# Optimization experiments

Hardware: AMD Instinct MI355X
Metric: run time of the kernel (lower is better)

The kernel has to match this reference:

```python
import jax, jax.numpy as jnp
import numpy as np

# Code / decoder configuration (regular (3,6) QC-LDPC, rate 1/2)
B, N, M, E, ITERS = 128, 24576, 12288, 73728, 10
CN_DEG = 6          # check-node degree (E = M * CN_DEG, and each VN has degree 3)
CLIP = 20.0         # clip_llr (q_bit == 0 -> clamp with straight-through gradient)
BIG = jnp.float32(1e30)  # acts as +inf for segment-min init


def _quantize(llr):
    """q_bit == 0: clamp to [-CLIP, CLIP] with straight-through estimator."""
    q = jnp.clip(llr, -CLIP, CLIP)
    return jax.lax.stop_gradient(q) + (llr - jax.lax.stop_gradient(llr))


def _decode(llr_in, cn_weight, ch_weight, cn_bias, edge_to_vn, edge_to_cn):
    c2v = jnp.zeros((B, E), jnp.float32)
    sum_llr = jnp.zeros((B, N), jnp.float32)
    dec = llr_in
    loss = jnp.float32(0.0)
    for it in range(ITERS):
        # --- channel weight (sharing[2] == 3: per-iteration scalar) ---
        w_ch = llr_in * ch_weight[it]
        # --- VN update: extrinsic sum at each variable node, gathered per edge ---
        v2c = _quantize(w_ch[:, edge_to_vn] + sum_llr[:, edge_to_vn] - c2v)
        # --- CN update (min-sum): per-CN sign parity + extrinsic min via min1/min2 ---
        a = jnp.abs(v2c)                      # [B, E]
        neg = v2c < 0
        parity = jnp.zeros((B, M), jnp.int32).at[:, edge_to_cn].add(neg.astype(jnp.int32)) % 2
        sign_tot = (1 - 2 * parity).astype(jnp.float32)          # [B, M]
        m1 = jnp.full((B, M), BIG, jnp.float32).at[:, edge_to_cn].min(a)
        is_min = a == m1[:, edge_to_cn]
        cnt = jnp.zeros((B, M), jnp.float32).at[:, edge_to_cn].add(is_min.astype(jnp.float32))
        m2 = jnp.full((B, M), BIG, jnp.float32).at[:, edge_to_cn].min(jnp.where(is_min, BIG, a))
        # edge is the unique minimum of its CN -> use second min; otherwise first min
        ext_min = jnp.where(is_min & (cnt[:, edge_to_cn] == 1.0), m2[:, edge_to_cn], m1[:, edge_to_cn])
        sign_e = 1.0 - 2.0 * neg.astype(jnp.float32)
        c2v_raw = sign_tot[:, edge_to_cn] * sign_e * ext_min
        # --- CN weight (sharing[0] == 3: per-iteration scalar) ---
        c2v_w = c2v_raw * cn_weight[it]
        # --- CN bias (offset): subtract from magnitude, negatives clipped to 0 ---
        mag = jax.nn.relu(jnp.abs(c2v_w) - cn_bias[it])
        c2v = _quantize(jnp.sign(c2v_w) * mag)
        # --- marginal accumulation + decision ---
        sum_llr = jnp.zeros((B, N), jnp.float32).at[:, edge_to_vn].add(c2v)
        dec = llr_in + sum_llr
        # BCE loss assuming all-zero codeword (bit 0 <-> positive LLR), multi-iter
        loss = loss + jnp.mean(jax.nn.softplus(-dec))
    return loss, dec


def setup_inputs() -> dict:
    key = jax.random.key(0)
    # AWGN-like channel LLRs for the all-zero codeword (mostly positive)
    llr_in = 2.0 + 2.0 * jax.random.normal(key, (B, N), dtype=jnp.float32)
    # Structured regular graph: edge e -> CN e // 6, edge e -> VN e % N
    edge_to_vn = jnp.arange(E, dtype=jnp.int32) % N    # each VN has degree 3
    edge_to_cn = jnp.arange(E, dtype=jnp.int32) // CN_DEG  # each CN has degree 6
    return {
        "llr_in": llr_in,
        "cn_weight": jnp.ones((ITERS,), jnp.float32),         # init_cn_weight = 1.0
        "ch_weight": jnp.ones((ITERS,), jnp.float32),         # init_ch_weight = 1.0
        "cn_bias": jnp.full((ITERS,), 0.3, jnp.float32),      # init_cn_bias = 0.3
        "edge_to_vn": edge_to_vn,
        "edge_to_cn": edge_to_cn,
    }


def reference(llr_in, cn_weight, ch_weight, cn_bias, edge_to_vn, edge_to_cn):
    return _decode(llr_in, cn_weight, ch_weight, cn_bias, edge_to_vn, edge_to_cn)
```

## Files before the change

### kernel.cpp

```cpp
#include <hip/hip_runtime.h>
#include <math.h>

#define B_     128
#define N_     24576
#define NCOMP_ 4096
#define ITERS_ 10
#define CLIP_  20.0f
#define NBLOCKS_ ((B_ * NCOMP_) / 256)


__device__ __forceinline__ float clipf(float x) {
    return fminf(fmaxf(x, -CLIP_), CLIP_);
}
__device__ __forceinline__ float clamp0c(float x) {
    return fminf(fmaxf(x, 0.f), CLIP_);
}

__global__ __launch_bounds__(256, 4) void ldpc_fused_kernel(
    const float* __restrict__ llr_in,
    const float* __restrict__ cn_weight,
    const float* __restrict__ ch_weight,
    const float* __restrict__ cn_bias,
    float* __restrict__ out,
    double* __restrict__ partials)
{
    const int gid = blockIdx.x * 256 + threadIdx.x;
    const int b = gid >> 12;
    const int k = gid & (NCOMP_ - 1);

    float cwv[ITERS_], cnwa[ITERS_], nbias[ITERS_];
    unsigned cnws[ITERS_];
#pragma unroll
    for (int i = 0; i < ITERS_; ++i) {
        float w = cn_weight[i];
        cwv[i]   = ch_weight[i];
        cnwa[i]  = fabsf(w);
        cnws[i]  = __float_as_uint(w) & 0x80000000u;
        nbias[i] = -cn_bias[i];
    }

    const float2* p2 = (const float2*)(llr_in + b * N_ + 6 * k);
    float2 t0 = p2[0], t1 = p2[1], t2 = p2[2];
    float llr[6] = {t0.x, t0.y, t1.x, t1.y, t2.x, t2.y};

    float c2v[3][6];
    float sum[6];
#pragma unroll
    for (int i = 0; i < 6; ++i) {
        sum[i] = 0.f;
        c2v[0][i] = 0.f; c2v[1][i] = 0.f; c2v[2][i] = 0.f;
    }

    float accMax = 0.f;
    float accLog = 0.f;

#pragma unroll
    for (int it = 0; it < ITERS_; ++it) {
        const float cw = cwv[it];

        float u6[6];
#pragma unroll
        for (int i = 0; i < 6; ++i) u6[i] = fmaf(llr[i], cw, sum[i]);

#pragma unroll
        for (int cn = 0; cn < 3; ++cn) {
            float t[6];
            unsigned tb[6];
            unsigned par = cnws[it];
#pragma unroll
            for (int j = 0; j < 6; ++j) {
                float v = clipf(u6[j] - c2v[cn][j]);
                t[j] = v;
                tb[j] = __float_as_uint(v);
                par ^= tb[j];
            }
            float a0 = fabsf(t[0]), a1 = fabsf(t[1]);
            float m1 = fminf(a0, a1);
            float m2 = fmaxf(a0, a1);
#pragma unroll
            for (int j = 2; j < 6; ++j) {
                float a = fabsf(t[j]);
                float mx = fmaxf(a, m1);
                m1 = fminf(m1, a);
                m2 = fminf(m2, mx);
            }
            float M1p = clamp0c(fmaf(m1, cnwa[it], nbias[it]));
            float M2p = clamp0c(fmaf(m2, cnwa[it], nbias[it]));
#pragma unroll
            for (int j = 0; j < 6; ++j) {
                float ext = (fabsf(t[j]) == m1) ? M2p : M1p;
                unsigned sgn = par ^ tb[j];
                c2v[cn][j] = __uint_as_float((sgn & 0x80000000u)
                                             | __float_as_uint(ext));
            }
        }

#pragma unroll
        for (int i = 0; i < 6; ++i) {
            sum[i] = (c2v[0][i] + c2v[1][i]) + c2v[2][i];
            float dec = llr[i] + sum[i];
            accMax += fmaxf(-dec, 0.f);
            accLog += __logf(1.f + __expf(-fabsf(dec)));
        }
    }

    float2* outd = (float2*)(out + 1 + b * N_ + 6 * k);
    outd[0] = make_float2(llr[0] + sum[0], llr[1] + sum[1]);
    outd[1] = make_float2(llr[2] + sum[2], llr[3] + sum[3]);
    outd[2] = make_float2(llr[4] + sum[4], llr[5] + sum[5]);

    float local_loss = accMax + accLog;
#pragma unroll
    for (int off = 32; off > 0; off >>= 1)
        local_loss += __shfl_down(local_loss, off);
    __shared__ float wsum[4];
    const int lane = threadIdx.x & 63;
    const int wid  = threadIdx.x >> 6;
    if (lane == 0) wsum[wid] = local_loss;
    __syncthreads();
    if (threadIdx.x == 0) {
        double t = ((double)wsum[0] + (double)wsum[1])
                 + ((double)wsum[2] + (double)wsum[3]);
        partials[blockIdx.x] = t;
    }
}

__global__ __launch_bounds__(256) void ldpc_finalize_kernel(
    const double* __restrict__ partials,
    float* __restrict__ out)
{
    double s = 0.0;
#pragma unroll
    for (int i = 0; i < NBLOCKS_ / 256; ++i)
        s += partials[threadIdx.x + 256 * i];
#pragma unroll
    for (int off = 32; off > 0; off >>= 1)
        s += __shfl_down(s, off);
    __shared__ double wsum[4];
    const int lane = threadIdx.x & 63;
    const int wid  = threadIdx.x >> 6;
    if (lane == 0) wsum[wid] = s;
    __syncthreads();
    if (threadIdx.x == 0) {
        double total = (wsum[0] + wsum[1]) + (wsum[2] + wsum[3]);
        out[0] = (float)(total * (1.0 / ((double)B_ * (double)N_)));
    }
}

extern "C" void kernel_launch(void* const* d_in, const int* in_sizes, int n_in,
                              void* d_out, int out_size, void* d_ws, size_t ws_size,
                              hipStream_t stream) {
    const float* llr_in    = (const float*)d_in[0];
    const float* cn_weight = (const float*)d_in[1];
    const float* ch_weight = (const float*)d_in[2];
    const float* cn_bias   = (const float*)d_in[3];

    float*  out      = (float*)d_out;
    double* partials = (double*)d_ws;

    ldpc_fused_kernel<<<NBLOCKS_, 256, 0, stream>>>(
        llr_in, cn_weight, ch_weight, cn_bias, out, partials);
    ldpc_finalize_kernel<<<1, 256, 0, stream>>>(partials, out);
}
```

Baseline: 102.1 us.

## Use min3/med3 min-sum, product-of-logs softplus, uniform scalar weights

Computes the first and second minimum of each check node with min3/med3 over two triples instead of a sequential compare chain. The softplus log terms are accumulated as a running product with a single log at the end, which removes 59 of the 60 log evaluations per thread. Weight loads are made wave-uniform with readfirstlane, and the occupancy hint rises from 4 to 6 waves. The product of up to 60 factors, each at most 2, stays within float range, but it trades per-term log accuracy for one log of a large product.

```diff
diff --git a/kernel.cpp b/kernel.cpp
--- a/kernel.cpp
+++ b/kernel.cpp
@@ -15,8 +15,17 @@
 __device__ __forceinline__ float clamp0c(float x) {
     return fminf(fmaxf(x, 0.f), CLIP_);
 }
+__device__ __forceinline__ float fmin3(float a, float b, float c) {
+    return fminf(fminf(a, b), c);
+}
+__device__ __forceinline__ float fmed3(float a, float b, float c) {
+    return __builtin_amdgcn_fmed3f(a, b, c);
+}
+__device__ __forceinline__ float rfl(float x) {
+    return __uint_as_float(__builtin_amdgcn_readfirstlane(__float_as_uint(x)));
+}
 
-__global__ __launch_bounds__(256, 4) void ldpc_fused_kernel(
+__global__ __launch_bounds__(256, 6) void ldpc_fused_kernel(
     const float* __restrict__ llr_in,
     const float* __restrict__ cn_weight,
     const float* __restrict__ ch_weight,
@@ -32,11 +41,11 @@
     unsigned cnws[ITERS_];
 #pragma unroll
     for (int i = 0; i < ITERS_; ++i) {
-        float w = cn_weight[i];
-        cwv[i]   = ch_weight[i];
+        float w  = rfl(cn_weight[i]);
+        cwv[i]   = rfl(ch_weight[i]);
         cnwa[i]  = fabsf(w);
         cnws[i]  = __float_as_uint(w) & 0x80000000u;
-        nbias[i] = -cn_bias[i];
+        nbias[i] = -rfl(cn_bias[i]);
     }
 
     const float2* p2 = (const float2*)(llr_in + b * N_ + 6 * k);
@@ -51,8 +60,8 @@
         c2v[0][i] = 0.f; c2v[1][i] = 0.f; c2v[2][i] = 0.f;
     }
 
-    float accMax = 0.f;
-    float accLog = 0.f;
+    float accMax  = 0.f;
+    float prodLog = 1.f;
 
 #pragma unroll
     for (int it = 0; it < ITERS_; ++it) {
@@ -65,32 +74,25 @@
 #pragma unroll
         for (int cn = 0; cn < 3; ++cn) {
             float t[6];
-            unsigned tb[6];
             unsigned par = cnws[it];
 #pragma unroll
             for (int j = 0; j < 6; ++j) {
-                float v = clipf(u6[j] - c2v[cn][j]);
-                t[j] = v;
-                tb[j] = __float_as_uint(v);
-                par ^= tb[j];
+                t[j] = clipf(u6[j] - c2v[cn][j]);
+                par ^= __float_as_uint(t[j]);
             }
-            float a0 = fabsf(t[0]), a1 = fabsf(t[1]);
-            float m1 = fminf(a0, a1);
-            float m2 = fmaxf(a0, a1);
-#pragma unroll
-            for (int j = 2; j < 6; ++j) {
-                float a = fabsf(t[j]);
-                float mx = fmaxf(a, m1);
-                m1 = fminf(m1, a);
-                m2 = fminf(m2, mx);
-            }
+            float minA = fmin3(fabsf(t[0]), fabsf(t[1]), fabsf(t[2]));
+            float medA = fmed3(fabsf(t[0]), fabsf(t[1]), fabsf(t[2]));
+            float minB = fmin3(fabsf(t[3]), fabsf(t[4]), fabsf(t[5]));
+            float medB = fmed3(fabsf(t[3]), fabsf(t[4]), fabsf(t[5]));
+            float m1 = fminf(minA, minB);
+            float m2 = fmin3(fmaxf(minA, minB), medA, medB);
             float M1p = clamp0c(fmaf(m1, cnwa[it], nbias[it]));
             float M2p = clamp0c(fmaf(m2, cnwa[it], nbias[it]));
 #pragma unroll
             for (int j = 0; j < 6; ++j) {
                 float ext = (fabsf(t[j]) == m1) ? M2p : M1p;
-                unsigned sgn = par ^ tb[j];
-                c2v[cn][j] = __uint_as_float((sgn & 0x80000000u)
+                unsigned sx = par ^ __float_as_uint(t[j]);
+                c2v[cn][j] = __uint_as_float((sx & 0x80000000u)
                                              | __float_as_uint(ext));
             }
         }
@@ -99,8 +101,8 @@
         for (int i = 0; i < 6; ++i) {
             sum[i] = (c2v[0][i] + c2v[1][i]) + c2v[2][i];
             float dec = llr[i] + sum[i];
-            accMax += fmaxf(-dec, 0.f);
-            accLog += __logf(1.f + __expf(-fabsf(dec)));
+            accMax  += fmaxf(-dec, 0.f);
+            prodLog *= 1.f + __expf(-fabsf(dec));
         }
     }
 
@@ -109,7 +111,7 @@
     outd[1] = make_float2(llr[2] + sum[2], llr[3] + sum[3]);
     outd[2] = make_float2(llr[4] + sum[4], llr[5] + sum[5]);
 
-    float local_loss = accMax + accLog;
+    float local_loss = accMax + __logf(prodLog);
 #pragma unroll
     for (int off = 32; off > 0; off >>= 1)
         local_loss += __shfl_down(local_loss, off);
```

After: 89.93 us. -11.9%, faster.
